# Performance work log

Hardware: AMD Instinct MI355X
Metric: run time of the kernel (lower is better)

The kernel has to match this reference:

```python
import jax, jax.numpy as jnp
import numpy as np
from jax import lax

B, H2, W2 = 16, 28, 28
INPUT_SIZE = (224, 224)
NUM_NEIGHBORS = 9
SIGMA = 4.0
KS = 2 * int(4.0 * SIGMA + 0.5) + 1  # kornia default kernel size = 33


def setup_inputs() -> dict:
    key = jax.random.key(0)
    k1, k2, k3 = jax.random.split(key, 3)
    return {
        "feat_layer2": jax.random.normal(k1, (B, 512, 28, 28), dtype=jnp.float32),
        "feat_layer3": jax.random.normal(k2, (B, 1024, 14, 14), dtype=jnp.float32),
        "memory_bank": jax.random.normal(k3, (16384, 1536), dtype=jnp.float32),
    }


def avg_pool3(x):
    # torch.nn.AvgPool2d(3, 1, 1) with count_include_pad=True: sum over 3x3 window
    # (zero padded) divided by 9 everywhere.
    s = lax.reduce_window(x, 0.0, lax.add, (1, 1, 3, 3), (1, 1, 1, 1),
                          [(0, 0), (0, 0), (1, 1), (1, 1)])
    return s / 9.0


def gaussian_kernel1d(ks, sigma):
    x = jnp.arange(ks, dtype=jnp.float32) - (ks - 1) / 2.0
    g = jnp.exp(-0.5 * (x / sigma) ** 2)
    return g / g.sum()


def gaussian_blur(x, k1d):
    # separable depthwise blur on [B,1,H,W], reflect padding (kornia default)
    ks = k1d.shape[0]
    p = ks // 2
    xp = jnp.pad(x, ((0, 0), (0, 0), (p, p), (p, p)), mode="reflect")
    kh = k1d.reshape(1, 1, ks, 1)
    kw = k1d.reshape(1, 1, 1, ks)
    dn = ("NCHW", "OIHW", "NCHW")
    xp = lax.conv_general_dilated(xp, kh, (1, 1), [(0, 0), (0, 0)], dimension_numbers=dn)
    xp = lax.conv_general_dilated(xp, kw, (1, 1), [(0, 0), (0, 0)], dimension_numbers=dn)
    return xp


def reference(feat_layer2, feat_layer3, memory_bank):
    # 1. local average pooling of each feature map
    f2 = avg_pool3(feat_layer2)            # [B,512,28,28]
    f3 = avg_pool3(feat_layer3)            # [B,1024,14,14]
    # 2. generate_embedding: nearest-upsample layer3 to layer2 spatial size, concat channels
    f3_up = jnp.repeat(jnp.repeat(f3, 2, axis=2), 2, axis=3)  # [B,1024,28,28]
    embedding = jnp.concatenate([f2, f3_up], axis=1)           # [B,1536,28,28]
    D = embedding.shape[1]
    # 3. reshape_embedding: [B,C,H,W] -> [B*H*W, C]
    emb = embedding.transpose(0, 2, 3, 1).reshape(-1, D)       # [N, D]
    # 4. nearest_neighbors: cdist (p=2) against memory bank + smallest-k
    x2 = jnp.sum(emb * emb, axis=1, keepdims=True)             # [N,1]
    m2 = jnp.sum(memory_bank * memory_bank, axis=1)            # [M]
    d2 = x2 + m2[None, :] - 2.0 * emb @ memory_bank.T          # [N,M]
    dist = jnp.sqrt(jnp.maximum(d2, 1e-12))
    neg_topk, _ = lax.top_k(-dist, NUM_NEIGHBORS)
    patch_scores = -neg_topk                                   # [N, k] ascending
    # 5. anomaly map: nearest-neighbor distance per patch, upsampled + blurred
    amap = patch_scores[:, 0].reshape(B, 1, H2, W2)
    scale = INPUT_SIZE[0] // H2
    amap = jnp.repeat(jnp.repeat(amap, scale, axis=2), scale, axis=3)  # nearest interp
    amap = gaussian_blur(amap, gaussian_kernel1d(KS, SIGMA))           # [B,1,224,224]
    # 6. anomaly score with softmax confidence reweighting (PatchCore Eq. 6)
    s0 = patch_scores[:, 0]
    max_idx = jnp.argmax(s0)
    confidence = patch_scores[max_idx]                                  # [k]
    weights = 1.0 - jnp.max(jnp.exp(confidence)) / jnp.sum(jnp.exp(confidence))
    anomaly_score = weights * jnp.max(s0)
    return amap, anomaly_score
```

## Files before the change

kernel.cpp:

```cpp
#include <hip/hip_runtime.h>
#include <hip/hip_bf16.h>

typedef __attribute__((ext_vector_type(4))) float f32x4;
typedef __attribute__((ext_vector_type(8))) short short8;
typedef __attribute__((ext_vector_type(4))) unsigned short u16x4;
typedef __attribute__((ext_vector_type(2))) unsigned short u16x2;

#define M_ROWS 12544
#define N_MEM  16384
#define K_DIM  1536

__device__ __forceinline__ float bf2f(unsigned short u) {
  return __uint_as_float(((unsigned)u) << 16);
}
__device__ __forceinline__ unsigned short f2bf(float f) {
  unsigned u = __float_as_uint(f);
  u += 0x7FFF + ((u >> 16) & 1);
  return (unsigned short)(u >> 16);
}

__global__ __launch_bounds__(256) void pool2_kernel(
    const float* __restrict__ f2, unsigned short* __restrict__ emb)
{
  int sq = blockIdx.x, cb = blockIdx.y, b = blockIdx.z;
  int h0 = sq * 7;
  __shared__ unsigned short tile[196][66];
  const float* base = f2 + ((size_t)b * 512 + cb * 64) * 784;
  #pragma unroll 2
  for (int i = 0; i < 49; ++i) {
    int idx = i * 256 + threadIdx.x;
    int cl = idx / 196;
    int p = idx - cl * 196;
    int hr = p / 28;
    int w = p - hr * 28;
    int h = h0 + hr;
    const float* plane = base + (size_t)cl * 784;
    float v = 0.f;
    #pragma unroll
    for (int dh = -1; dh <= 1; ++dh) {
      int hh = h + dh; if (hh < 0 || hh > 27) continue;
      #pragma unroll
      for (int dw = -1; dw <= 1; ++dw) {
        int ww = w + dw; if (ww < 0 || ww > 27) continue;
        v += plane[hh * 28 + ww];
      }
    }
    tile[p][cl] = f2bf(v * (1.f / 9.f));
  }
  __syncthreads();
  #pragma unroll 2
  for (int i = 0; i < 49; ++i) {
    int idx = i * 256 + threadIdx.x;
    int s = idx >> 6, c = idx & 63;
    int r = b * 784 + h0 * 28 + s;
    emb[(size_t)r * K_DIM + cb * 64 + c] = tile[s][c];
  }
}

__global__ __launch_bounds__(256) void pool3_kernel(
    const float* __restrict__ f3, unsigned short* __restrict__ emb)
{
  int cb = blockIdx.x, b = blockIdx.y;
  __shared__ unsigned short tile[196][66];
  const float* base = f3 + ((size_t)b * 1024 + cb * 64) * 196;
  #pragma unroll 2
  for (int i = 0; i < 49; ++i) {
    int idx = i * 256 + threadIdx.x;
    int cl = idx / 196;
    int p = idx - cl * 196;
    int h3 = p / 14;
    int w3 = p - h3 * 14;
    const float* plane = base + (size_t)cl * 196;
    float v = 0.f;
    #pragma unroll
    for (int dh = -1; dh <= 1; ++dh) {
      int hh = h3 + dh; if (hh < 0 || hh > 13) continue;
      #pragma unroll
      for (int dw = -1; dw <= 1; ++dw) {
        int ww = w3 + dw; if (ww < 0 || ww > 13) continue;
        v += plane[hh * 14 + ww];
      }
    }
    tile[p][cl] = f2bf(v * (1.f / 9.f));
  }
  __syncthreads();
  #pragma unroll 2
  for (int i = 0; i < 98; ++i) {
    int idx = i * 256 + threadIdx.x;
    int s = idx >> 5;
    int cp = (idx & 31) * 2;
    int h = s / 28, w = s - (s / 28) * 28;
    int p = (h >> 1) * 14 + (w >> 1);
    u16x2 v = *(const u16x2*)&tile[p][cp];
    *(u16x2*)&emb[(size_t)(b * 784 + s) * K_DIM + 512 + cb * 64 + cp] = v;
  }
}

__global__ __launch_bounds__(256) void mbconv_kernel(
    const float* __restrict__ mb, unsigned short* __restrict__ mbb,
    float* __restrict__ m2)
{
  int wave = threadIdx.x >> 6, lane = threadIdx.x & 63;
  int row = blockIdx.x * 4 + wave;
  const float* src = mb + (size_t)row * K_DIM;
  unsigned short* dst = mbb + (size_t)row * K_DIM;
  float s = 0.f;
  #pragma unroll
  for (int c = 0; c < 6; ++c) {
    int off = c * 256 + lane * 4;
    float4 v = *(const float4*)(src + off);
    s += v.x * v.x + v.y * v.y + v.z * v.z + v.w * v.w;
    u16x4 o; o[0] = f2bf(v.x); o[1] = f2bf(v.y); o[2] = f2bf(v.z); o[3] = f2bf(v.w);
    *(u16x4*)(dst + off) = o;
  }
  #pragma unroll
  for (int d = 1; d < 64; d <<= 1) s += __shfl_xor(s, d);
  if (lane == 0) m2[row] = s;
}

__global__ __launch_bounds__(256) void x2_kernel(
    const unsigned short* __restrict__ emb, float* __restrict__ x2)
{
  int wave = threadIdx.x >> 6, lane = threadIdx.x & 63;
  int row = blockIdx.x * 4 + wave;
  const unsigned short* src = emb + (size_t)row * K_DIM;
  float s = 0.f;
  #pragma unroll
  for (int c = 0; c < 3; ++c) {
    short8 v = *(const short8*)(src + c * 512 + lane * 8);
    #pragma unroll
    for (int j = 0; j < 8; ++j) {
      float f = bf2f((unsigned short)v[j]);
      s += f * f;
    }
  }
  #pragma unroll
  for (int d = 1; d < 64; d <<= 1) s += __shfl_xor(s, d);
  if (lane == 0) x2[row] = s;
}

__global__ __launch_bounds__(256) void gemm_min_kernel(
    const unsigned short* __restrict__ A,
    const unsigned short* __restrict__ Bm,
    const float* __restrict__ m2,
    float* __restrict__ partial)
{
  __shared__ unsigned short lA[128 * 32];
  __shared__ unsigned short lB[128 * 32];
  const int tid = threadIdx.x;
  const int wave = tid >> 6, lane = tid & 63;
  const int bn = blockIdx.x, bm = blockIdx.y;
  const int rowBase = bm * 128, colBase = bn * 128;
  const int wr = wave >> 1, wc = wave & 1;

  f32x4 acc[4][4];
  #pragma unroll
  for (int i = 0; i < 4; ++i)
    #pragma unroll
    for (int j = 0; j < 4; ++j)
      acc[i][j] = (f32x4){0.f, 0.f, 0.f, 0.f};

  for (int kk = 0; kk < K_DIM; kk += 32) {
    #pragma unroll
    for (int i = 0; i < 2; ++i) {
      int e = i * 2048 + wave * 512 + lane * 8;
      int trow = e >> 5, tcol = e & 31;
      __builtin_amdgcn_global_load_lds(
          (const __attribute__((address_space(1))) void*)(A + (size_t)(rowBase + trow) * K_DIM + kk + tcol),
          (__attribute__((address_space(3))) void*)(lA + i * 2048 + wave * 512), 16, 0, 0);
      __builtin_amdgcn_global_load_lds(
          (const __attribute__((address_space(1))) void*)(Bm + (size_t)(colBase + trow) * K_DIM + kk + tcol),
          (__attribute__((address_space(3))) void*)(lB + i * 2048 + wave * 512), 16, 0, 0);
    }
    __syncthreads();
    short8 af[4], bf[4];
    #pragma unroll
    for (int f = 0; f < 4; ++f) {
      af[f] = *reinterpret_cast<const short8*>(&lA[(wr * 64 + f * 16 + (lane & 15)) * 32 + (lane >> 4) * 8]);
      bf[f] = *reinterpret_cast<const short8*>(&lB[(wc * 64 + f * 16 + (lane & 15)) * 32 + (lane >> 4) * 8]);
    }
    #pragma unroll
    for (int i = 0; i < 4; ++i)
      #pragma unroll
      for (int j = 0; j < 4; ++j)
        acc[i][j] = __builtin_amdgcn_mfma_f32_16x16x32_bf16(af[i], bf[j], acc[i][j], 0, 0, 0);
    __syncthreads();
  }

  float m2v[4];
  #pragma unroll
  for (int j = 0; j < 4; ++j)
    m2v[j] = m2[colBase + wc * 64 + j * 16 + (lane & 15)];
  const int q = lane >> 4;
  #pragma unroll
  for (int i = 0; i < 4; ++i) {
    #pragma unroll
    for (int v = 0; v < 4; ++v) {
      float mn = fminf(fminf(m2v[0] - 2.f * acc[i][0][v], m2v[1] - 2.f * acc[i][1][v]),
                       fminf(m2v[2] - 2.f * acc[i][2][v], m2v[3] - 2.f * acc[i][3][v]));
      #pragma unroll
      for (int d = 1; d < 16; d <<= 1) mn = fminf(mn, __shfl_xor(mn, d));
      if ((lane & 15) == 0) {
        int r = rowBase + wr * 64 + i * 16 + q * 4 + v;
        partial[(size_t)r * 256 + bn * 2 + wc] = mn;
      }
    }
  }
}

__global__ __launch_bounds__(256) void reduce_min_kernel(
    const float* __restrict__ partial, const float* __restrict__ x2,
    float* __restrict__ s0)
{
  int wave = threadIdx.x >> 6, lane = threadIdx.x & 63;
  int r = blockIdx.x * 4 + wave;
  float4 v4 = *(const float4*)&partial[(size_t)r * 256 + lane * 4];
  float mn = fminf(fminf(v4.x, v4.y), fminf(v4.z, v4.w));
  #pragma unroll
  for (int d = 1; d < 64; d <<= 1) mn = fminf(mn, __shfl_xor(mn, d));
  if (lane == 0) s0[r] = sqrtf(fmaxf(x2[r] + mn, 1e-12f));
}

__global__ __launch_bounds__(1024) void argmax_kernel(
    const float* __restrict__ s0, float* __restrict__ scal)
{
  __shared__ float sv[1024];
  __shared__ int si[1024];
  int tid = threadIdx.x;
  float best = -1e30f; int bi = 0x7fffffff;
  for (int i = tid; i < M_ROWS; i += 1024) {
    float v = s0[i];
    if (v > best) { best = v; bi = i; }
  }
  sv[tid] = best; si[tid] = bi;
  __syncthreads();
  for (int s = 512; s > 0; s >>= 1) {
    if (tid < s) {
      if (sv[tid + s] > sv[tid] || (sv[tid + s] == sv[tid] && si[tid + s] < si[tid])) {
        sv[tid] = sv[tid + s]; si[tid] = si[tid + s];
      }
    }
    __syncthreads();
  }
  if (tid == 0) { scal[0] = sv[0]; ((int*)scal)[1] = si[0]; }
}

__global__ __launch_bounds__(256) void rowdist_kernel(
    const unsigned short* __restrict__ emb, const unsigned short* __restrict__ mbb,
    const float* __restrict__ x2, const float* __restrict__ m2,
    const float* __restrict__ scal, float* __restrict__ dists)
{
  int wave = threadIdx.x >> 6, lane = threadIdx.x & 63;
  int m = blockIdx.x * 4 + wave;
  int ridx = ((const int*)scal)[1];
  const unsigned short* er = emb + (size_t)ridx * K_DIM;
  const unsigned short* mr = mbb + (size_t)m * K_DIM;
  float dot = 0.f;
  #pragma unroll
  for (int c = 0; c < 3; ++c) {
    short8 a = *(const short8*)(er + c * 512 + lane * 8);
    short8 b = *(const short8*)(mr + c * 512 + lane * 8);
    #pragma unroll
    for (int j = 0; j < 8; ++j)
      dot += bf2f((unsigned short)a[j]) * bf2f((unsigned short)b[j]);
  }
  #pragma unroll
  for (int d = 1; d < 64; d <<= 1) dot += __shfl_xor(dot, d);
  if (lane == 0)
    dists[m] = sqrtf(fmaxf(x2[ridx] + m2[m] - 2.f * dot, 1e-12f));
}

__global__ __launch_bounds__(1024) void topk_kernel(
    const float* __restrict__ dists, const float* __restrict__ scal,
    float* __restrict__ out)
{
  __shared__ float conf[9];
  __shared__ int chosen[9];
  __shared__ float swv[16];
  __shared__ int swi[16];
  int tid = threadIdx.x, lane = tid & 63, wave = tid >> 6;
  for (int t = 0; t < 9; ++t) {
    float best = 1e30f; int bi = 0x7fffffff;
    for (int i = tid; i < N_MEM; i += 1024) {
      bool skip = false;
      for (int u = 0; u < t; ++u) skip = skip || (chosen[u] == i);
      if (skip) continue;
      float v = dists[i];
      if (v < best || (v == best && i < bi)) { best = v; bi = i; }
    }
    #pragma unroll
    for (int d = 1; d < 64; d <<= 1) {
      float ov = __shfl_xor(best, d); int oi = __shfl_xor(bi, d);
      if (ov < best || (ov == best && oi < bi)) { best = ov; bi = oi; }
    }
    if (lane == 0) { swv[wave] = best; swi[wave] = bi; }
    __syncthreads();
    if (tid == 0) {
      float bb = swv[0]; int bbi = swi[0];
      for (int w = 1; w < 16; ++w)
        if (swv[w] < bb || (swv[w] == bb && swi[w] < bbi)) { bb = swv[w]; bbi = swi[w]; }
      conf[t] = bb; chosen[t] = bbi;
    }
    __syncthreads();
  }
  if (tid == 0) {
    float me = conf[0];
    for (int i = 1; i < 9; ++i) me = fmaxf(me, conf[i]);
    float den = 0.f;
    for (int i = 0; i < 9; ++i) den += expf(conf[i] - me);
    float w = 1.f - 1.f / den;
    out[802816] = w * scal[0];
  }
}

__global__ __launch_bounds__(256) void blurV_kernel(
    const float* __restrict__ s0, float* __restrict__ tmp)
{
  __shared__ float g[33];
  __shared__ float ginv;
  int tid = threadIdx.x;
  if (tid < 33) { float x = (tid - 16) * 0.25f; g[tid] = expf(-0.5f * x * x); }
  __syncthreads();
  if (tid == 0) { float s = 0.f; for (int i = 0; i < 33; ++i) s += g[i]; ginv = 1.f / s; }
  __syncthreads();
  int gid = blockIdx.x * 256 + tid;
  int b = gid / 50176;
  int rem = gid - b * 50176;
  int y = rem / 224, x = rem - (rem / 224) * 224;
  const float* sb = s0 + b * 784;
  int sx = x >> 3;
  float acc = 0.f;
  for (int k = 0; k < 33; ++k) {
    int yy = y + k - 16;
    yy = (yy < 0) ? -yy : yy;
    yy = (yy > 223) ? 446 - yy : yy;
    acc += g[k] * sb[(yy >> 3) * 28 + sx];
  }
  tmp[gid] = acc * ginv;
}

__global__ __launch_bounds__(256) void blurH_kernel(
    const float* __restrict__ tmp, float* __restrict__ out)
{
  __shared__ float g[33];
  __shared__ float ginv;
  int tid = threadIdx.x;
  if (tid < 33) { float x = (tid - 16) * 0.25f; g[tid] = expf(-0.5f * x * x); }
  __syncthreads();
  if (tid == 0) { float s = 0.f; for (int i = 0; i < 33; ++i) s += g[i]; ginv = 1.f / s; }
  __syncthreads();
  int gid = blockIdx.x * 256 + tid;
  int b = gid / 50176;
  int rem = gid - b * 50176;
  int y = rem / 224, x = rem - (rem / 224) * 224;
  const float* tb = tmp + b * 50176 + y * 224;
  float acc = 0.f;
  for (int k = 0; k < 33; ++k) {
    int xx = x + k - 16;
    xx = (xx < 0) ? -xx : xx;
    xx = (xx > 223) ? 446 - xx : xx;
    acc += g[k] * tb[xx];
  }
  out[gid] = acc * ginv;
}

extern "C" void kernel_launch(void* const* d_in, const int* in_sizes, int n_in,
                              void* d_out, int out_size, void* d_ws, size_t ws_size,
                              hipStream_t stream) {
  const float* f2 = (const float*)d_in[0];
  const float* f3 = (const float*)d_in[1];
  const float* mb = (const float*)d_in[2];
  float* out = (float*)d_out;
  char* ws = (char*)d_ws;

  unsigned short* emb = (unsigned short*)(ws + 0);
  unsigned short* mbb = (unsigned short*)(ws + 38535168);
  float* x2      = (float*)(ws + 88866816);
  float* m2      = (float*)(ws + 88916992);
  float* partial = (float*)(ws + 88982528);
  float* s0      = (float*)(ws + 101827584);
  float* scal    = (float*)(ws + 101877760);
  float* dists   = (float*)(ws + 101877824);
  float* tmp     = (float*)(ws + 101943360);

  hipLaunchKernelGGL(pool2_kernel, dim3(4, 8, 16), dim3(256), 0, stream, f2, emb);
  hipLaunchKernelGGL(pool3_kernel, dim3(16, 16), dim3(256), 0, stream, f3, emb);
  hipLaunchKernelGGL(mbconv_kernel, dim3(4096), dim3(256), 0, stream, mb, mbb, m2);
  hipLaunchKernelGGL(x2_kernel, dim3(3136), dim3(256), 0, stream, emb, x2);
  hipLaunchKernelGGL(gemm_min_kernel, dim3(128, 98), dim3(256), 0, stream, emb, mbb, m2, partial);
  hipLaunchKernelGGL(reduce_min_kernel, dim3(3136), dim3(256), 0, stream, partial, x2, s0);
  hipLaunchKernelGGL(argmax_kernel, dim3(1), dim3(1024), 0, stream, s0, scal);
  hipLaunchKernelGGL(rowdist_kernel, dim3(4096), dim3(256), 0, stream, emb, mbb, x2, m2, scal, dists);
  hipLaunchKernelGGL(topk_kernel, dim3(1), dim3(1024), 0, stream, dists, scal, out);
  hipLaunchKernelGGL(blurV_kernel, dim3(3136), dim3(256), 0, stream, s0, tmp);
  hipLaunchKernelGGL(blurH_kernel, dim3(3136), dim3(256), 0, stream, tmp, out);
}
```

Measured before the change: 1.234 ms.

## Enlarge GEMM tiles to 256x256 with triple-buffered async LDS pipeline and swizzle

Rewrites the fused distance GEMM to use 256x256 output tiles per 512-thread block, with 8x4 MFMA fragments per wave. Global-to-LDS loads are staged two k-tiles ahead in a three-slot ring, using explicit vmcnt waits and a single barrier per k-step, so memory latency overlaps with MFMA work. An XOR swizzle on LDS columns reduces bank conflicts. The cost is higher register use and 96KB of LDS per block, which limits occupancy. The grid also shrinks to 3136 blocks, and the partial-min layout changes to four column groups per tile.

```diff
diff --git a/kernel.cpp b/kernel.cpp
--- a/kernel.cpp
+++ b/kernel.cpp
@@ -9,6 +9,7 @@
 #define M_ROWS 12544
 #define N_MEM  16384
 #define K_DIM  1536
+#define NT     48
 
 __device__ __forceinline__ float bf2f(unsigned short u) {
   return __uint_as_float(((unsigned)u) << 16);
@@ -139,70 +140,95 @@
   if (lane == 0) x2[row] = s;
 }
 
-__global__ __launch_bounds__(256) void gemm_min_kernel(
+__global__ __launch_bounds__(512, 2) void gemm_min_kernel(
     const unsigned short* __restrict__ A,
     const unsigned short* __restrict__ Bm,
     const float* __restrict__ m2,
     float* __restrict__ partial)
 {
-  __shared__ unsigned short lA[128 * 32];
-  __shared__ unsigned short lB[128 * 32];
+  __shared__ unsigned short lds[49152];
   const int tid = threadIdx.x;
   const int wave = tid >> 6, lane = tid & 63;
   const int bn = blockIdx.x, bm = blockIdx.y;
-  const int rowBase = bm * 128, colBase = bn * 128;
-  const int wr = wave >> 1, wc = wave & 1;
-
-  f32x4 acc[4][4];
-  #pragma unroll
-  for (int i = 0; i < 4; ++i)
+  const int rowBase = bm * 256, colBase = bn * 256;
+  const int wr = wave >> 2, wn = wave & 3;
+  const int l15 = lane & 15, q = lane >> 4;
+  const int sq = (q ^ ((l15 >> 1) & 3)) << 3;
+
+  const int stRow = tid >> 2;
+  const int scol = ((tid & 3) ^ ((stRow >> 1) & 3)) << 3;
+  const unsigned short* gA0 = A + (size_t)(rowBase + stRow) * K_DIM + scol;
+  const unsigned short* gA1 = gA0 + (size_t)128 * K_DIM;
+  const unsigned short* gB0 = Bm + (size_t)(colBase + stRow) * K_DIM + scol;
+  const unsigned short* gB1 = gB0 + (size_t)128 * K_DIM;
+  const int ldsW = wave * 512;
+
+  f32x4 acc[8][4];
+  #pragma unroll
+  for (int i = 0; i < 8; ++i)
     #pragma unroll
     for (int j = 0; j < 4; ++j)
       acc[i][j] = (f32x4){0.f, 0.f, 0.f, 0.f};
 
-  for (int kk = 0; kk < K_DIM; kk += 32) {
-    #pragma unroll
-    for (int i = 0; i < 2; ++i) {
-      int e = i * 2048 + wave * 512 + lane * 8;
-      int trow = e >> 5, tcol = e & 31;
-      __builtin_amdgcn_global_load_lds(
-          (const __attribute__((address_space(1))) void*)(A + (size_t)(rowBase + trow) * K_DIM + kk + tcol),
-          (__attribute__((address_space(3))) void*)(lA + i * 2048 + wave * 512), 16, 0, 0);
-      __builtin_amdgcn_global_load_lds(
-          (const __attribute__((address_space(1))) void*)(Bm + (size_t)(colBase + trow) * K_DIM + kk + tcol),
-          (__attribute__((address_space(3))) void*)(lB + i * 2048 + wave * 512), 16, 0, 0);
-    }
-    __syncthreads();
-    short8 af[4], bf[4];
-    #pragma unroll
-    for (int f = 0; f < 4; ++f) {
-      af[f] = *reinterpret_cast<const short8*>(&lA[(wr * 64 + f * 16 + (lane & 15)) * 32 + (lane >> 4) * 8]);
-      bf[f] = *reinterpret_cast<const short8*>(&lB[(wc * 64 + f * 16 + (lane & 15)) * 32 + (lane >> 4) * 8]);
-    }
-    #pragma unroll
-    for (int i = 0; i < 4; ++i)
-      #pragma unroll
-      for (int j = 0; j < 4; ++j)
-        acc[i][j] = __builtin_amdgcn_mfma_f32_16x16x32_bf16(af[i], bf[j], acc[i][j], 0, 0, 0);
-    __syncthreads();
-  }
+#define GLL(src, dstoff) __builtin_amdgcn_global_load_lds( \
+    (const __attribute__((address_space(1))) void*)(src), \
+    (__attribute__((address_space(3))) void*)(lds + (dstoff)), 16, 0, 0)
+
+#define STAGE(slot, kk) do { \
+    GLL(gA0 + (kk), (slot) * 8192 + ldsW); \
+    GLL(gA1 + (kk), (slot) * 8192 + 4096 + ldsW); \
+    GLL(gB0 + (kk), 24576 + (slot) * 8192 + ldsW); \
+    GLL(gB1 + (kk), 24576 + (slot) * 8192 + 4096 + ldsW); \
+  } while (0)
+
+  STAGE(0, 0);
+  STAGE(1, 32);
+  asm volatile("s_waitcnt vmcnt(4)\n\ts_barrier" ::: "memory");
+
+#define KTILE(slot, stslot, t) do { \
+    if ((t) + 2 < NT) STAGE(stslot, ((t) + 2) * 32); \
+    const unsigned short* Ab = lds + (slot) * 8192; \
+    const unsigned short* Bb = lds + 24576 + (slot) * 8192; \
+    short8 af[8], bf[4]; \
+    _Pragma("unroll") \
+    for (int j = 0; j < 4; ++j) \
+      bf[j] = *(const short8*)(Bb + (wn * 64 + j * 16 + l15) * 32 + sq); \
+    _Pragma("unroll") \
+    for (int i = 0; i < 8; ++i) \
+      af[i] = *(const short8*)(Ab + (wr * 128 + i * 16 + l15) * 32 + sq); \
+    _Pragma("unroll") \
+    for (int i = 0; i < 8; ++i) \
+      _Pragma("unroll") \
+      for (int j = 0; j < 4; ++j) \
+        acc[i][j] = __builtin_amdgcn_mfma_f32_16x16x32_bf16(af[i], bf[j], acc[i][j], 0, 0, 0); \
+    if ((t) + 2 < NT) { asm volatile("s_waitcnt vmcnt(4)\n\ts_barrier" ::: "memory"); } \
+    else             { asm volatile("s_waitcnt vmcnt(0)\n\ts_barrier" ::: "memory"); } \
+  } while (0)
+
+  for (int tb = 0; tb < NT; tb += 3) {
+    KTILE(0, 2, tb);
+    KTILE(1, 0, tb + 1);
+    KTILE(2, 1, tb + 2);
+  }
+#undef KTILE
+#undef STAGE
+#undef GLL
 
   float m2v[4];
   #pragma unroll
   for (int j = 0; j < 4; ++j)
-    m2v[j] = m2[colBase + wc * 64 + j * 16 + (lane & 15)];
-  const int q = lane >> 4;
-  #pragma unroll
-  for (int i = 0; i < 4; ++i) {
+    m2v[j] = m2[colBase + wn * 64 + j * 16 + l15];
+  #pragma unroll
+  for (int i = 0; i < 8; ++i) {
     #pragma unroll
     for (int v = 0; v < 4; ++v) {
       float mn = fminf(fminf(m2v[0] - 2.f * acc[i][0][v], m2v[1] - 2.f * acc[i][1][v]),
                        fminf(m2v[2] - 2.f * acc[i][2][v], m2v[3] - 2.f * acc[i][3][v]));
       #pragma unroll
       for (int d = 1; d < 16; d <<= 1) mn = fminf(mn, __shfl_xor(mn, d));
-      if ((lane & 15) == 0) {
-        int r = rowBase + wr * 64 + i * 16 + q * 4 + v;
-        partial[(size_t)r * 256 + bn * 2 + wc] = mn;
+      if (l15 == 0) {
+        int r = rowBase + wr * 128 + i * 16 + q * 4 + v;
+        partial[(size_t)r * 256 + bn * 4 + wn] = mn;
       }
     }
   }
@@ -387,7 +413,7 @@
   hipLaunchKernelGGL(pool3_kernel, dim3(16, 16), dim3(256), 0, stream, f3, emb);
   hipLaunchKernelGGL(mbconv_kernel, dim3(4096), dim3(256), 0, stream, mb, mbb, m2);
   hipLaunchKernelGGL(x2_kernel, dim3(3136), dim3(256), 0, stream, emb, x2);
-  hipLaunchKernelGGL(gemm_min_kernel, dim3(128, 98), dim3(256), 0, stream, emb, mbb, m2, partial);
+  hipLaunchKernelGGL(gemm_min_kernel, dim3(64, 49), dim3(512), 0, stream, emb, mbb, m2, partial);
   hipLaunchKernelGGL(reduce_min_kernel, dim3(3136), dim3(256), 0, stream, partial, x2, s0);
   hipLaunchKernelGGL(argmax_kernel, dim3(1), dim3(1024), 0, stream, s0, scal);
   hipLaunchKernelGGL(rowdist_kernel, dim3(4096), dim3(256), 0, stream, emb, mbb, x2, m2, scal, dists);
```

Result: faster. 1.070 ms (-13.3%).
